# Optimization experiments

Hardware: AMD Instinct MI355X
Metric: run time of the kernel (lower is better)

Reference implementation:

```python
import jax, jax.numpy as jnp
import numpy as np

N_ENS = 4        # number of FGL sub-layers
B, N_IN, N_OUT = 1, 16384, 4096
IN_C, OUT_C = 16, 16
DENSITY = 0.10   # sparsity proxy for A + dA random perturbation


def setup_inputs() -> dict:
    key = jax.random.key(0)
    kx, ka, km, kw, kb = jax.random.split(key, 5)
    x = jax.random.normal(kx, (B, N_IN, IN_C), dtype=jnp.float32)
    # Dense storage of the n perturbed sparse adjacencies A_i (n_out, n_in)
    A_vals = jax.random.normal(ka, (N_ENS, N_OUT, N_IN), dtype=jnp.float32)
    A_mask = jax.random.bernoulli(km, DENSITY, (N_ENS, N_OUT, N_IN))
    As = A_vals * A_mask.astype(jnp.float32)
    Ws = jax.random.normal(kw, (N_ENS, IN_C, OUT_C), dtype=jnp.float32) * (1.0 / np.sqrt(IN_C))
    bs = jax.random.normal(kb, (N_ENS, OUT_C), dtype=jnp.float32) * 0.01
    return {"x": x, "As": As, "Ws": Ws, "bs": bs}


def reference(x, As, Ws, bs):
    # Each FGL_i: y_i = (A_i @ x) @ W_i + b_i
    # x: [b, n_in, f]; As: [n, n_out, n_in]; Ws: [n, f, g]; bs: [n, g]
    h = jnp.einsum('noi,bif->nbof', As, x)            # graph aggregation per ensemble member
    y = jnp.einsum('nbof,nfg->nbog', h, Ws)           # per-member linear transform
    y = y + bs[:, None, None, :]
    return jnp.mean(y, axis=0)                        # sum over n members / n
```

## Files before the change

### kernel.cpp

```cpp
#include <hip/hip_runtime.h>


#define N_ENS 4
#define N_OUT 4096
#define N_IN  16384
#define ROWS  (N_ENS * N_OUT)
#define GSPLIT 32
#define ICHUNK (N_IN / GSPLIT)

__global__ __launch_bounds__(256, 6) void k_main(const float* __restrict__ A,
                                                 const float* __restrict__ x,
                                                 float* __restrict__ hp) {
    const int split  = blockIdx.x & (GSPLIT - 1);
    const int rowblk = blockIdx.x >> 5;
    const int row = rowblk * 256 + threadIdx.x;
    const int i0 = split * ICHUNK;

    const float* Ap  = A + (size_t)row * N_IN + i0;
    const float* xp0 = x + (size_t)i0 * 16;

    float acc[16];
#pragma unroll
    for (int f = 0; f < 16; ++f) acc[f] = 0.0f;

    for (int s = 0; s < ICHUNK / 16; ++s) {
        float4 av4[4];
#pragma unroll
        for (int q = 0; q < 4; ++q)
            av4[q] = *(const float4*)(Ap + s * 16 + q * 4);
        const float* af = (const float*)av4;
        const float* xp = xp0 + (size_t)s * 256;

#pragma unroll
        for (int ii = 0; ii < 16; ++ii) {
            const float av = af[ii];
#pragma unroll
            for (int f = 0; f < 16; ++f)
                acc[f] = fmaf(av, xp[ii * 16 + f], acc[f]);
        }
    }

    float* outp = hp + ((size_t)split * ROWS + row) * 16;
#pragma unroll
    for (int f = 0; f < 16; ++f) outp[f] = acc[f];
}

__global__ __launch_bounds__(256) void k_hsum(const float* __restrict__ hp,
                                              float* __restrict__ h) {
    int t = blockIdx.x * 256 + threadIdx.x;
    float s = 0.0f;
#pragma unroll
    for (int sp = 0; sp < GSPLIT; ++sp)
        s += hp[(size_t)sp * (ROWS * 16) + t];
    h[t] = s;
}

__global__ __launch_bounds__(256) void k_out(const float* __restrict__ h,
                                             const float* __restrict__ Ws,
                                             const float* __restrict__ bs,
                                             float* __restrict__ out) {
    __shared__ float Wsm[N_ENS * 16 * 16];
    __shared__ float bsm[N_ENS * 16];
    int tid = threadIdx.x;
#pragma unroll
    for (int r = 0; r < 4; ++r) Wsm[tid + 256 * r] = Ws[tid + 256 * r];
    if (tid < 64) bsm[tid] = bs[tid];
    __syncthreads();

    int idx = blockIdx.x * 256 + tid;
    int o = idx >> 4;
    int gg = idx & 15;
    float s = 0.0f;
#pragma unroll
    for (int n = 0; n < N_ENS; ++n) {
        const float* hr = h + ((size_t)(n * N_OUT + o) << 4);
        float t = 0.0f;
#pragma unroll
        for (int f = 0; f < 16; ++f)
            t = fmaf(hr[f], Wsm[n * 256 + f * 16 + gg], t);
        s += t + bsm[n * 16 + gg];
    }
    out[idx] = 0.25f * s;
}

extern "C" void kernel_launch(void* const* d_in, const int* in_sizes, int n_in,
                              void* d_out, int out_size, void* d_ws, size_t ws_size,
                              hipStream_t stream) {
    const float* x  = (const float*)d_in[0];
    const float* As = (const float*)d_in[1];
    const float* Ws = (const float*)d_in[2];
    const float* bs = (const float*)d_in[3];
    float* out = (float*)d_out;

    float* hp = (float*)d_ws;
    float* h  = (float*)((char*)d_ws + (size_t)32 * 1024 * 1024);

    k_main<<<64 * GSPLIT, 256, 0, stream>>>(As, x, hp);
    k_hsum<<<(ROWS * 16) / 256, 256, 0, stream>>>(hp, h);
    k_out<<<(N_OUT * 16) / 256, 256, 0, stream>>>(h, Ws, bs, out);
}
```

Before: 1.415 ms.

## Stage x chunk in LDS, double-buffer A loads, vectorize split reduction

The main kernel now copies its 512x16 slice of x into shared memory once per block and reads it from LDS instead of global memory. Loads of A rows are double-buffered across two register sets so the next 16 values arrive while the current ones are multiplied. The partial-sum reduction kernel now reads and writes float4 and launches a quarter as many threads. In exchange the kernel uses 32 KB of LDS per block and more registers, and occupancy hints drop from 6 to 4 blocks per CU.

Result: no change. 1.420 ms (+0.4%).

```diff
diff --git a/kernel.cpp b/kernel.cpp
--- a/kernel.cpp
+++ b/kernel.cpp
@@ -8,50 +8,74 @@
 #define GSPLIT 32
 #define ICHUNK (N_IN / GSPLIT)
 
-__global__ __launch_bounds__(256, 6) void k_main(const float* __restrict__ A,
+__global__ __launch_bounds__(256, 4) void k_main(const float* __restrict__ A,
                                                  const float* __restrict__ x,
                                                  float* __restrict__ hp) {
     const int split  = blockIdx.x & (GSPLIT - 1);
     const int rowblk = blockIdx.x >> 5;
-    const int row = rowblk * 256 + threadIdx.x;
-    const int i0 = split * ICHUNK;
+    const int tid    = threadIdx.x;
+    const int row    = rowblk * 256 + tid;
+    const int i0     = split * ICHUNK;
 
-    const float* Ap  = A + (size_t)row * N_IN + i0;
-    const float* xp0 = x + (size_t)i0 * 16;
+    __shared__ float xs[ICHUNK * 16];
+
+    {
+        const float4* xg = (const float4*)(x + (size_t)i0 * 16);
+        float4* xl = (float4*)xs;
+#pragma unroll
+        for (int q = 0; q < 8; ++q)
+            xl[tid + 256 * q] = xg[tid + 256 * q];
+    }
+    __syncthreads();
+
+    const float* Ap = A + (size_t)row * N_IN + i0;
 
     float acc[16];
 #pragma unroll
     for (int f = 0; f < 16; ++f) acc[f] = 0.0f;
 
-    for (int s = 0; s < ICHUNK / 16; ++s) {
-        float4 av4[4];
+#define COMPUTE(buf, sbase) do {                                         \
+        const float* af_ = (const float*)(buf);                          \
+        const float* xp_ = xs + (sbase) * 256;                           \
+        _Pragma("unroll")                                                \
+        for (int ii = 0; ii < 16; ++ii) {                                \
+            const float av_ = af_[ii];                                   \
+            _Pragma("unroll")                                            \
+            for (int f = 0; f < 16; ++f)                                 \
+                acc[f] = fmaf(av_, xp_[ii * 16 + f], acc[f]);            \
+        }                                                                \
+    } while (0)
+
+    float4 aA[4], aB[4];
 #pragma unroll
-        for (int q = 0; q < 4; ++q)
-            av4[q] = *(const float4*)(Ap + s * 16 + q * 4);
-        const float* af = (const float*)av4;
-        const float* xp = xp0 + (size_t)s * 256;
+    for (int q = 0; q < 4; ++q) aA[q] = ((const float4*)Ap)[q];
 
+    for (int s = 0; s < ICHUNK / 16; s += 2) {
 #pragma unroll
-        for (int ii = 0; ii < 16; ++ii) {
-            const float av = af[ii];
+        for (int q = 0; q < 4; ++q) aB[q] = ((const float4*)(Ap + (s + 1) * 16))[q];
+        COMPUTE(aA, s);
+        if (s + 2 < ICHUNK / 16) {
 #pragma unroll
-            for (int f = 0; f < 16; ++f)
-                acc[f] = fmaf(av, xp[ii * 16 + f], acc[f]);
+            for (int q = 0; q < 4; ++q) aA[q] = ((const float4*)(Ap + (s + 2) * 16))[q];
         }
+        COMPUTE(aB, s + 1);
     }
+#undef COMPUTE
 
     float* outp = hp + ((size_t)split * ROWS + row) * 16;
 #pragma unroll
     for (int f = 0; f < 16; ++f) outp[f] = acc[f];
 }
 
-__global__ __launch_bounds__(256) void k_hsum(const float* __restrict__ hp,
-                                              float* __restrict__ h) {
+__global__ __launch_bounds__(256) void k_hsum(const float4* __restrict__ hp,
+                                              float4* __restrict__ h) {
     int t = blockIdx.x * 256 + threadIdx.x;
-    float s = 0.0f;
+    float4 s; s.x = 0.f; s.y = 0.f; s.z = 0.f; s.w = 0.f;
 #pragma unroll
-    for (int sp = 0; sp < GSPLIT; ++sp)
-        s += hp[(size_t)sp * (ROWS * 16) + t];
+    for (int sp = 0; sp < GSPLIT; ++sp) {
+        float4 v = hp[(size_t)sp * (ROWS * 4) + t];
+        s.x += v.x; s.y += v.y; s.z += v.z; s.w += v.w;
+    }
     h[t] = s;
 }
 
@@ -96,6 +120,6 @@
     float* h  = (float*)((char*)d_ws + (size_t)32 * 1024 * 1024);
 
     k_main<<<64 * GSPLIT, 256, 0, stream>>>(As, x, hp);
-    k_hsum<<<(ROWS * 16) / 256, 256, 0, stream>>>(hp, h);
+    k_hsum<<<(ROWS * 16 / 4) / 256, 256, 0, stream>>>((const float4*)hp, (float4*)h);
     k_out<<<(N_OUT * 16) / 256, 256, 0, stream>>>(h, Ws, bs, out);
 }
```

## Stage A tiles into LDS via async global_load_lds with double buffering

Applied to the files above, without the earlier changes.

Reworks the main aggregation kernel so each wave streams 64-row by 128-column tiles of A into LDS using direct global-to-LDS loads, with an XOR swizzle and a double buffer so the next tile's loads overlap compute on the current one. The input split drops from 32 to 4, the block shrinks to 128 threads, and the reduction kernel is vectorised to float4. The aim is to get coalesced, overlapped streaming of the large A matrix instead of strided per-thread row loads. In exchange it uses 128KB of LDS per block, which limits occupancy to one block per CU, and the grid shrinks to 512 blocks.

Result: slower. 2.056 ms (+45.3%).

```diff
diff --git a/kernel.cpp b/kernel.cpp
--- a/kernel.cpp
+++ b/kernel.cpp
@@ -5,53 +5,96 @@
 #define N_OUT 4096
 #define N_IN  16384
 #define ROWS  (N_ENS * N_OUT)
-#define GSPLIT 32
-#define ICHUNK (N_IN / GSPLIT)
+#define SPLITS 4
+#define KCH   (N_IN / SPLITS)
+#define TI    128
+#define NT    (KCH / TI)
+#define TROWS 64
 
-__global__ __launch_bounds__(256, 6) void k_main(const float* __restrict__ A,
-                                                 const float* __restrict__ x,
-                                                 float* __restrict__ hp) {
-    const int split  = blockIdx.x & (GSPLIT - 1);
-    const int rowblk = blockIdx.x >> 5;
-    const int row = rowblk * 256 + threadIdx.x;
-    const int i0 = split * ICHUNK;
+__global__ __launch_bounds__(128) void k_main(const float* __restrict__ A,
+                                              const float* __restrict__ x,
+                                              float* __restrict__ hp) {
+    __shared__ float smem[2 * 2 * 8192];
 
-    const float* Ap  = A + (size_t)row * N_IN + i0;
-    const float* xp0 = x + (size_t)i0 * 16;
+    const int split = blockIdx.x & (SPLITS - 1);
+    const int rowg  = blockIdx.x >> 2;
+    const int wave  = threadIdx.x >> 6;
+    const int lane  = threadIdx.x & 63;
+    const int i0    = split * KCH;
+    const int row0  = rowg * 128 + wave * TROWS;
+
+    float* lds = smem + wave * 16384;
+    const float* Aw = A + (size_t)row0 * N_IN + i0;
+
+#define STAGE(buf, t) do {                                                    \
+        const float* Asrc = Aw + (size_t)(t) * TI;                            \
+        _Pragma("unroll")                                                     \
+        for (int k = 0; k < 32; ++k) {                                        \
+            const int r = 2 * k + (lane >> 5);                                \
+            const int j = (lane & 31) ^ (r & 7);        \
+            const float* src = Asrc + (size_t)r * N_IN + j * 4;               \
+            __builtin_amdgcn_global_load_lds(                                 \
+                (const __attribute__((address_space(1))) void*)src,           \
+                (__attribute__((address_space(3))) void*)&lds[(buf) * 8192 + k * 256], \
+                16, 0, 0);                                                    \
+        }                                                                     \
+    } while (0)
+
+#define COMPUTE(buf, t) do {                                                  \
+        const float* xpt = x + (size_t)(i0 + (t) * TI) * 16;                  \
+        _Pragma("unroll")                                                     \
+        for (int c = 0; c < 4; ++c) {                                         \
+            float4 a4[8];                                                     \
+            _Pragma("unroll")                                                 \
+            for (int e = 0; e < 8; ++e)                                       \
+                a4[e] = *(const float4*)&lds[(buf) * 8192 + lane * 128 +      \
+                                             (c * 8 + (e ^ (lane & 7))) * 4]; \
+            const float* af = (const float*)a4;          \
+            const float* xp = xpt + (size_t)c * 512;                          \
+            _Pragma("unroll")                                                 \
+            for (int ii = 0; ii < 32; ++ii) {                                 \
+                const float av = af[ii];                                      \
+                _Pragma("unroll")                                             \
+                for (int f = 0; f < 16; ++f)                                  \
+                    acc[f] = fmaf(av, xp[ii * 16 + f], acc[f]);               \
+            }                                                                 \
+        }                                                                     \
+    } while (0)
 
     float acc[16];
 #pragma unroll
     for (int f = 0; f < 16; ++f) acc[f] = 0.0f;
 
-    for (int s = 0; s < ICHUNK / 16; ++s) {
-        float4 av4[4];
-#pragma unroll
-        for (int q = 0; q < 4; ++q)
-            av4[q] = *(const float4*)(Ap + s * 16 + q * 4);
-        const float* af = (const float*)av4;
-        const float* xp = xp0 + (size_t)s * 256;
+    STAGE(0, 0);
 
-#pragma unroll
-        for (int ii = 0; ii < 16; ++ii) {
-            const float av = af[ii];
-#pragma unroll
-            for (int f = 0; f < 16; ++f)
-                acc[f] = fmaf(av, xp[ii * 16 + f], acc[f]);
+    for (int t = 0; t < NT; ++t) {
+        if (t + 1 < NT) {
+            STAGE((t + 1) & 1, t + 1);
+            asm volatile("s_waitcnt vmcnt(32)" ::: "memory");
+        } else {
+            asm volatile("s_waitcnt vmcnt(0)" ::: "memory");
         }
+        __builtin_amdgcn_sched_barrier(0);
+        COMPUTE(t & 1, t);
     }
+#undef STAGE
+#undef COMPUTE
 
+    const int row = row0 + lane;
     float* outp = hp + ((size_t)split * ROWS + row) * 16;
 #pragma unroll
     for (int f = 0; f < 16; ++f) outp[f] = acc[f];
 }
 
-__global__ __launch_bounds__(256) void k_hsum(const float* __restrict__ hp,
-                                              float* __restrict__ h) {
+__global__ __launch_bounds__(256) void k_hsum(const float4* __restrict__ hp,
+                                              float4* __restrict__ h) {
     int t = blockIdx.x * 256 + threadIdx.x;
-    float s = 0.0f;
+    float4 s; s.x = 0.f; s.y = 0.f; s.z = 0.f; s.w = 0.f;
 #pragma unroll
-    for (int sp = 0; sp < GSPLIT; ++sp)
-        s += hp[(size_t)sp * (ROWS * 16) + t];
+    for (int sp = 0; sp < SPLITS; ++sp) {
+        float4 v = hp[(size_t)sp * (ROWS * 4) + t];
+        s.x += v.x; s.y += v.y; s.z += v.z; s.w += v.w;
+    }
     h[t] = s;
 }
 
@@ -95,7 +138,7 @@
     float* hp = (float*)d_ws;
     float* h  = (float*)((char*)d_ws + (size_t)32 * 1024 * 1024);
 
-    k_main<<<64 * GSPLIT, 256, 0, stream>>>(As, x, hp);
-    k_hsum<<<(ROWS * 16) / 256, 256, 0, stream>>>(hp, h);
+    k_main<<<128 * SPLITS, 128, 0, stream>>>(As, x, hp);
+    k_hsum<<<(ROWS * 16 / 4) / 256, 256, 0, stream>>>((const float4*)hp, (float4*)h);
     k_out<<<(N_OUT * 16) / 256, 256, 0, stream>>>(h, Ws, bs, out);
 }
```
